# Optimization experiments

Measured on AMD Instinct MI355X. Metric: run time of the kernel, lower is better.

The kernel has to match this reference:

```python
import jax, jax.numpy as jnp
import numpy as np

N = 40000; E = 500000; IN = 128; ED = 16; HID = 64; HEADS = 4; OUT = 256; B = 128
NEG = 0.2  # GATv2 leaky_relu negative slope


def _add_self_loops(edge_index, edge_attr, n):
    # PyG add_self_loops with fill_value='mean': loop attr = mean of incoming edge attrs per node
    dst = edge_index[1]
    s = jax.ops.segment_sum(edge_attr, dst, num_segments=n)
    c = jax.ops.segment_sum(jnp.ones((edge_attr.shape[0],), edge_attr.dtype), dst, num_segments=n)
    loop_attr = s / jnp.maximum(c, 1.0)[:, None]
    loops = jnp.arange(n, dtype=edge_index.dtype)
    ei = jnp.concatenate([edge_index, jnp.stack([loops, loops])], axis=1)
    ea = jnp.concatenate([edge_attr, loop_attr], axis=0)
    return ei, ea


def _seg_softmax(logits, seg, n):
    m = jax.ops.segment_max(logits, seg, num_segments=n)
    m = jnp.where(jnp.isfinite(m), m, 0.0)  # guard empty segments
    e = jnp.exp(logits - m[seg])
    z = jax.ops.segment_sum(e, seg, num_segments=n)
    return e / (z[seg] + 1e-16)


def _gatv2(x, src, dst, ea, Wl, bl, Wr, br, We, att, bias, heads, oc, concat):
    n = x.shape[0]
    xl = (x @ Wl + bl).reshape(n, heads, oc)  # lin_l (source/message transform)
    xr = (x @ Wr + br).reshape(n, heads, oc)  # lin_r (target transform)
    ef = (ea @ We).reshape(-1, heads, oc)     # lin_edge (no bias)
    s = jax.nn.leaky_relu(xl[src] + xr[dst] + ef, NEG)  # [Etot,H,C]
    alpha = _seg_softmax(jnp.einsum('ehc,hc->eh', s, att), dst, n)  # scatter-softmax over dst
    out = jax.ops.segment_sum(xl[src] * alpha[..., None], dst, num_segments=n)  # [N,H,C]
    out = out.reshape(n, heads * oc) if concat else out.mean(axis=1)
    return out + bias


def setup_inputs():
    ks = jax.random.split(jax.random.key(0), 32)
    W = lambda i, shp: jax.random.normal(ks[i], shp, jnp.float32) * 0.05
    z = lambda d: jnp.zeros((d,), jnp.float32)
    H = HEADS * HID
    return dict(
        x=jax.random.normal(ks[0], (N, IN), jnp.float32),
        edge_index=jax.random.randint(ks[1], (2, E), 0, N),
        edge_attr=jax.random.normal(ks[2], (E, ED), jnp.float32),
        batch=jnp.sort(jax.random.randint(ks[3], (N,), 0, B)),
        batch_size=B,
        c1_Wl=W(4, (IN, H)), c1_bl=z(H), c1_Wr=W(5, (IN, H)), c1_br=z(H), c1_We=W(6, (ED, H)), c1_att=W(7, (HEADS, HID)), c1_bias=z(H),
        c2_Wl=W(8, (H, H)), c2_bl=z(H), c2_Wr=W(9, (H, H)), c2_br=z(H), c2_We=W(10, (ED, H)), c2_att=W(11, (HEADS, HID)), c2_bias=z(H),
        c3_Wl=W(12, (H, OUT)), c3_bl=z(OUT), c3_Wr=W(13, (H, OUT)), c3_br=z(OUT), c3_We=W(14, (ED, OUT)), c3_att=W(15, (1, OUT)), c3_bias=z(OUT),
        gate_W1=W(16, (OUT, 128)), gate_b1=z(128), gate_W2=W(17, (128, 1)), gate_b2=z(1),
        reg_W1=W(18, (OUT, 128)), reg_b1=z(128), reg_W2=W(19, (128, 2)), reg_b2=z(2),
    )


def reference(x, edge_index, edge_attr, batch, batch_size,
              c1_Wl, c1_bl, c1_Wr, c1_br, c1_We, c1_att, c1_bias,
              c2_Wl, c2_bl, c2_Wr, c2_br, c2_We, c2_att, c2_bias,
              c3_Wl, c3_bl, c3_Wr, c3_br, c3_We, c3_att, c3_bias,
              gate_W1, gate_b1, gate_W2, gate_b2,
              reg_W1, reg_b1, reg_W2, reg_b2):
    # task_type='homo_lumo' path; dropout disabled (inference)
    ei, ea = _add_self_loops(edge_index, edge_attr, N)
    src, dst = ei[0], ei[1]
    h = jax.nn.relu(_gatv2(x, src, dst, ea, c1_Wl, c1_bl, c1_Wr, c1_br, c1_We, c1_att, c1_bias, HEADS, HID, True))
    h = jax.nn.relu(_gatv2(h, src, dst, ea, c2_Wl, c2_bl, c2_Wr, c2_br, c2_We, c2_att, c2_bias, HEADS, HID, True))
    h = _gatv2(h, src, dst, ea, c3_Wl, c3_bl, c3_Wr, c3_br, c3_We, c3_att, c3_bias, 1, OUT, True)
    # AttentionalAggregation pooling
    gate = jax.nn.relu(h @ gate_W1 + gate_b1) @ gate_W2 + gate_b2  # [N,1]
    a = _seg_softmax(gate[:, 0], batch, batch_size)
    g = jax.ops.segment_sum(h * a[:, None], batch, num_segments=batch_size)  # [B,OUT]
    return jax.nn.relu(g @ reg_W1 + reg_b1) @ reg_W2 + reg_b2  # [B,2]
```

## Files before the change

kernel.cpp:

```cpp
#include <hip/hip_runtime.h>
#include <math.h>

constexpr int N_NODES = 40000;
constexpr int N_EDGES = 500000;
constexpr int ETOT    = N_EDGES + N_NODES;
constexpr int IN_DIM  = 128;
constexpr int ED_DIM  = 16;
constexpr int FEAT    = 256;
constexpr int BATCH   = 128;
constexpr float NEG   = 0.2f;
constexpr int NCHUNK  = (N_NODES + 255) / 256;

typedef __bf16 bf16x8 __attribute__((ext_vector_type(8)));
typedef float  f32x4  __attribute__((ext_vector_type(4)));

__global__ __launch_bounds__(256) void k_deg(const int* __restrict__ dst, int* __restrict__ deg)
{
    int e = blockIdx.x * 256 + threadIdx.x;
    if (e >= ETOT) return;
    int v = e < N_EDGES ? dst[e] : e - N_EDGES;
    atomicAdd(&deg[v], 1);
}

__global__ __launch_bounds__(256) void k_scan1(const int* __restrict__ deg, int* __restrict__ bsum)
{
    __shared__ int s[256];
    int t = threadIdx.x;
    int idx = blockIdx.x * 256 + t;
    s[t] = idx < N_NODES ? deg[idx] : 0;
    __syncthreads();
    for (int st = 128; st; st >>= 1) { if (t < st) s[t] += s[t + st]; __syncthreads(); }
    if (t == 0) bsum[blockIdx.x] = s[0];
}

__global__ __launch_bounds__(256) void k_scan2(const int* __restrict__ bsum,
    int* __restrict__ boff, int* __restrict__ rowptr)
{
    __shared__ int s[256];
    int t = threadIdx.x;
    int v = t < NCHUNK ? bsum[t] : 0;
    s[t] = v;
    __syncthreads();
    for (int off = 1; off < 256; off <<= 1) {
        int x = (t >= off) ? s[t - off] : 0;
        __syncthreads();
        s[t] += x;
        __syncthreads();
    }
    if (t < NCHUNK) boff[t] = s[t] - v;
    if (t == 0) rowptr[N_NODES] = ETOT;
}

__global__ __launch_bounds__(256) void k_scan3(const int* __restrict__ deg,
    const int* __restrict__ boff, int* __restrict__ rowptr)
{
    __shared__ int s[256];
    int t = threadIdx.x;
    int idx = blockIdx.x * 256 + t;
    int v = idx < N_NODES ? deg[idx] : 0;
    s[t] = v;
    __syncthreads();
    for (int off = 1; off < 256; off <<= 1) {
        int x = (t >= off) ? s[t - off] : 0;
        __syncthreads();
        s[t] += x;
        __syncthreads();
    }
    if (idx < N_NODES) rowptr[idx] = boff[blockIdx.x] + s[t] - v;
}

__global__ __launch_bounds__(256) void k_fill(const int* __restrict__ srcA, const int* __restrict__ dst,
    const int* __restrict__ rowptr, int* __restrict__ fill, int2* __restrict__ elist2)
{
    int e = blockIdx.x * 256 + threadIdx.x;
    if (e >= ETOT) return;
    int v = e < N_EDGES ? dst[e]  : e - N_EDGES;
    int s = e < N_EDGES ? srcA[e] : e - N_EDGES;
    int pos = rowptr[v] + atomicAdd(&fill[v], 1);
    elist2[pos] = make_int2(s, e);
}

__global__ __launch_bounds__(256) void k_loop_csr(const int2* __restrict__ elist2,
    const int* __restrict__ rowptr, const float* __restrict__ ea, float* __restrict__ loop_attr)
{
    int t = blockIdx.x * 256 + threadIdx.x;
    if (t >= N_NODES * ED_DIM) return;
    int n = t >> 4, d = t & 15;
    int p0 = rowptr[n], p1 = rowptr[n + 1];
    float s = 0.f; int c = 0;
    for (int p = p0; p < p1; ++p) {
        int e = elist2[p].y;
        if (e < N_EDGES) { s += ea[(size_t)e * ED_DIM + d]; ++c; }
    }
    loop_attr[t] = s / (float)(c > 0 ? c : 1);
}

__device__ __forceinline__ void bsplit(float x, unsigned short& h, unsigned short& l)
{
    unsigned u = __float_as_uint(x);
    unsigned r = (u + 0x7FFFu + ((u >> 16) & 1u)) >> 16;
    h = (unsigned short)r;
    float rem = x - __uint_as_float(r << 16);
    unsigned u2 = __float_as_uint(rem);
    l = (unsigned short)((u2 + 0x7FFFu + ((u2 >> 16) & 1u)) >> 16);
}

__global__ __launch_bounds__(256) void k_cvt(const float* __restrict__ X,
    unsigned short* __restrict__ Xh, unsigned short* __restrict__ Xl, int n4)
{
    int i = blockIdx.x * 256 + threadIdx.x;
    if (i >= n4) return;
    float4 v = ((const float4*)X)[i];
    ushort4 h, l;
    bsplit(v.x, h.x, l.x);
    bsplit(v.y, h.y, l.y);
    bsplit(v.z, h.z, l.z);
    bsplit(v.w, h.w, l.w);
    ((ushort4*)Xh)[i] = h;
    ((ushort4*)Xl)[i] = l;
}

__global__ __launch_bounds__(256) void k_cvtT(const float* __restrict__ W,
    unsigned short* __restrict__ WhT, unsigned short* __restrict__ WlT, int K, int N)
{
    int i = blockIdx.x * 256 + threadIdx.x;
    if (i >= K * N) return;
    int k = i / N, n = i - k * N;
    unsigned short h, l;
    bsplit(W[i], h, l);
    WhT[(size_t)n * K + k] = h;
    WlT[(size_t)n * K + k] = l;
}


__device__ __forceinline__ void stage16(const unsigned short* g, void* lds)
{
#if __has_builtin(__builtin_amdgcn_global_load_lds)
    __builtin_amdgcn_global_load_lds(
        (const __attribute__((address_space(1))) void*)g,
        (__attribute__((address_space(3))) void*)lds, 16, 0, 0);
#else
    ((uint4*)lds)[threadIdx.x & 63] = *(const uint4*)g;
#endif
}

__global__ __launch_bounds__(256) void k_mgemm(
    const unsigned short* __restrict__ Ah, const unsigned short* __restrict__ Al,
    const unsigned short* __restrict__ BhT, const unsigned short* __restrict__ BlT,
    const float* __restrict__ bias, float* __restrict__ C,
    int M, int N, int K, int act)
{
    __shared__ uint4 sAh[512], sAl[512], sBh[512], sBl[512];

    int t = threadIdx.x;
    int lane = t & 63;
    int w = t >> 6;
    int mh = w >> 1, nh = w & 1;
    int bm = blockIdx.x * 128, bn = blockIdx.y * 128;
    int q = lane >> 4, lm = lane & 15;

    int ar0 = bm + w * 16 + lm;        ar0 = ar0 < M ? ar0 : M - 1;
    int ar1 = bm + (w + 4) * 16 + lm;  ar1 = ar1 < M ? ar1 : M - 1;
    int bc0 = bn + w * 16 + lm;
    int bc1 = bn + (w + 4) * 16 + lm;
    size_t aoff0 = (size_t)ar0 * K + q * 8;
    size_t aoff1 = (size_t)ar1 * K + q * 8;
    size_t boff0 = (size_t)bc0 * K + q * 8;
    size_t boff1 = (size_t)bc1 * K + q * 8;

    f32x4 acc[4][4] = {};

    int nk = K >> 5;
    for (int ks = 0; ks < nk; ++ks) {
        int k0 = ks << 5;
        if (ks) __syncthreads();
        stage16(Ah  + aoff0 + k0, &sAh[w * 64]);
        stage16(Ah  + aoff1 + k0, &sAh[(w + 4) * 64]);
        stage16(Al  + aoff0 + k0, &sAl[w * 64]);
        stage16(Al  + aoff1 + k0, &sAl[(w + 4) * 64]);
        stage16(BhT + boff0 + k0, &sBh[w * 64]);
        stage16(BhT + boff1 + k0, &sBh[(w + 4) * 64]);
        stage16(BlT + boff0 + k0, &sBl[w * 64]);
        stage16(BlT + boff1 + k0, &sBl[(w + 4) * 64]);
        __syncthreads();

        bf16x8 fah[4], fal[4], fbh[4], fbl[4];
        #pragma unroll
        for (int mt = 0; mt < 4; ++mt) {
            fah[mt] = __builtin_bit_cast(bf16x8, sAh[(mh * 4 + mt) * 64 + lane]);
            fal[mt] = __builtin_bit_cast(bf16x8, sAl[(mh * 4 + mt) * 64 + lane]);
        }
        #pragma unroll
        for (int nt = 0; nt < 4; ++nt) {
            fbh[nt] = __builtin_bit_cast(bf16x8, sBh[(nh * 4 + nt) * 64 + lane]);
            fbl[nt] = __builtin_bit_cast(bf16x8, sBl[(nh * 4 + nt) * 64 + lane]);
        }
        #pragma unroll
        for (int mt = 0; mt < 4; ++mt)
            #pragma unroll
            for (int nt = 0; nt < 4; ++nt) {
                acc[mt][nt] = __builtin_amdgcn_mfma_f32_16x16x32_bf16(fah[mt], fbh[nt], acc[mt][nt], 0, 0, 0);
                acc[mt][nt] = __builtin_amdgcn_mfma_f32_16x16x32_bf16(fah[mt], fbl[nt], acc[mt][nt], 0, 0, 0);
                acc[mt][nt] = __builtin_amdgcn_mfma_f32_16x16x32_bf16(fal[mt], fbh[nt], acc[mt][nt], 0, 0, 0);
            }
    }

    #pragma unroll
    for (int nt = 0; nt < 4; ++nt) {
        int col = bn + nh * 64 + nt * 16 + lm;
        float bb = bias[col];
        #pragma unroll
        for (int mt = 0; mt < 4; ++mt) {
            #pragma unroll
            for (int i = 0; i < 4; ++i) {
                int row = bm + mh * 64 + mt * 16 + q * 4 + i;
                if (row < M) {
                    float o = acc[mt][nt][i] + bb;
                    if (act) o = fmaxf(o, 0.f);
                    C[(size_t)row * N + col] = o;
                }
            }
        }
    }
}

static void launch_mgemm(const unsigned short* Ah, const unsigned short* Al,
                         const unsigned short* BhT, const unsigned short* BlT,
                         const float* bias, float* C, int M, int N, int K, int act,
                         hipStream_t stream)
{
    dim3 grid((M + 127) / 128, N / 128);
    k_mgemm<<<grid, 256, 0, stream>>>(Ah, Al, BhT, BlT, bias, C, M, N, K, act);
}

#define XELOAD(s) do {                                                                \
    int src_ = __builtin_amdgcn_readfirstlane(eS[s].x);                               \
    int e_   = __builtin_amdgcn_readfirstlane(eS[s].y);                               \
    const float4* eb4_ = reinterpret_cast<const float4*>(                             \
        (e_ < N_EDGES) ? ea + (size_t)e_ * ED_DIM                                     \
                       : loop_attr + (size_t)src_ * ED_DIM);                          \
    evS[s][0] = eb4_[0]; evS[s][1] = eb4_[1];                                         \
    evS[s][2] = eb4_[2]; evS[s][3] = eb4_[3];                                         \
    xlvS[s] = *(const float4*)(xl + (size_t)src_ * FEAT + base);                      \
} while (0)

#define COMPUTE(s) do {                                                               \
    float ef0_ = 0.f, ef1_ = 0.f, ef2_ = 0.f, ef3_ = 0.f;                             \
    const float* ed_ = (const float*)evS[s];                                          \
    _Pragma("unroll")                                                                 \
    for (int d_ = 0; d_ < ED_DIM; ++d_) {                                             \
        float a_ = ed_[d_];                                                           \
        ef0_ = fmaf(a_, weR[d_].x, ef0_); ef1_ = fmaf(a_, weR[d_].y, ef1_);           \
        ef2_ = fmaf(a_, weR[d_].z, ef2_); ef3_ = fmaf(a_, weR[d_].w, ef3_);           \
    }                                                                                 \
    float s0_ = xlvS[s].x + xrv.x + ef0_;                                             \
    float s1_ = xlvS[s].y + xrv.y + ef1_;                                             \
    float s2_ = xlvS[s].z + xrv.z + ef2_;                                             \
    float s3_ = xlvS[s].w + xrv.w + ef3_;                                             \
    s0_ = fmaxf(s0_, 0.f) + NEG * fminf(s0_, 0.f);                                    \
    s1_ = fmaxf(s1_, 0.f) + NEG * fminf(s1_, 0.f);                                    \
    s2_ = fmaxf(s2_, 0.f) + NEG * fminf(s2_, 0.f);                                    \
    s3_ = fmaxf(s3_, 0.f) + NEG * fminf(s3_, 0.f);                                    \
    float l_ = fmaf(s0_, attR.x, fmaf(s1_, attR.y, fmaf(s2_, attR.z, s3_ * attR.w))); \
    l_ += __shfl_xor(l_, 1, 64);                                                      \
    l_ += __shfl_xor(l_, 2, 64);                                                      \
    l_ += __shfl_xor(l_, 4, 64);                                                      \
    l_ += __shfl_xor(l_, 8, 64);                                                      \
    if (H == 1) { l_ += __shfl_xor(l_, 16, 64); l_ += __shfl_xor(l_, 32, 64); }       \
    float nm_ = fmaxf(m, l_);                                                         \
    float sc_ = __expf(m - nm_);                                                      \
    float w_  = __expf(l_ - nm_);                                                     \
    z = fmaf(z, sc_, w_);                                                             \
    m = nm_;                                                                          \
    acc.x = fmaf(acc.x, sc_, w_ * xlvS[s].x);                                         \
    acc.y = fmaf(acc.y, sc_, w_ * xlvS[s].y);                                         \
    acc.z = fmaf(acc.z, sc_, w_ * xlvS[s].z);                                         \
    acc.w = fmaf(acc.w, sc_, w_ * xlvS[s].w);                                         \
} while (0)

template <int H, int RELU, int OUTMODE>
__global__ __launch_bounds__(256, 4) void k_gat(
    const float* __restrict__ xl, const float* __restrict__ xr,
    const float* __restrict__ ea, const float* __restrict__ loop_attr,
    const int2* __restrict__ elist2, const int* __restrict__ rowptr,
    const float* __restrict__ We, const float* __restrict__ att,
    const float* __restrict__ bias, float* __restrict__ out,
    unsigned short* __restrict__ outH, unsigned short* __restrict__ outL)
{
    int t = threadIdx.x;
    int lane = t & 63;
    int n = __builtin_amdgcn_readfirstlane(blockIdx.x * 4 + (t >> 6));
    int base = lane * 4;

    float4 weR[ED_DIM];
    #pragma unroll
    for (int d = 0; d < ED_DIM; ++d)
        weR[d] = *(const float4*)(We + d * FEAT + base);

    float4 attR = *(const float4*)(att + base);
    float4 xrv  = *(const float4*)(xr + (size_t)n * FEAT + base);

    float m = -INFINITY, z = 0.f;
    float4 acc = {0.f, 0.f, 0.f, 0.f};

    int p0 = rowptr[n], p1 = rowptr[n + 1];
    int pe = p1 - 1;

    int2   eS[2];
    float4 evS[2][4];
    float4 xlvS[2];

    eS[0] = elist2[p0];
    { int pc = p0 + 1 > pe ? pe : p0 + 1; eS[1] = elist2[pc]; }
    XELOAD(0);

    int p = p0;
    while (true) {
        XELOAD(1);
        { int pn = p + 2 > pe ? pe : p + 2; eS[0] = elist2[pn]; }
        COMPUTE(0);
        if (++p >= p1) break;
        XELOAD(0);
        { int pn = p + 2 > pe ? pe : p + 2; eS[1] = elist2[pn]; }
        COMPUTE(1);
        if (++p >= p1) break;
    }

    float inv = 1.0f / (z + 1e-16f);
    float4 bs = *(const float4*)(bias + base);
    float4 o;
    o.x = fmaf(acc.x, inv, bs.x);
    o.y = fmaf(acc.y, inv, bs.y);
    o.z = fmaf(acc.z, inv, bs.z);
    o.w = fmaf(acc.w, inv, bs.w);
    if (RELU) {
        o.x = fmaxf(o.x, 0.f); o.y = fmaxf(o.y, 0.f);
        o.z = fmaxf(o.z, 0.f); o.w = fmaxf(o.w, 0.f);
    }
    if (OUTMODE == 2)
        *(float4*)(out + (size_t)n * FEAT + base) = o;
    ushort4 oh, ol;
    bsplit(o.x, oh.x, ol.x);
    bsplit(o.y, oh.y, ol.y);
    bsplit(o.z, oh.z, ol.z);
    bsplit(o.w, oh.w, ol.w);
    *(ushort4*)(outH + (size_t)n * FEAT + base) = oh;
    *(ushort4*)(outL + (size_t)n * FEAT + base) = ol;
}

__global__ __launch_bounds__(256) void k_gate_score(const float* __restrict__ ghid,
    const float* __restrict__ W2, const float* __restrict__ b2, float* __restrict__ gate)
{
    int lane = threadIdx.x & 63;
    int n = blockIdx.x * 4 + (threadIdx.x >> 6);
    float v = ghid[(size_t)n * 128 + lane] * W2[lane] + ghid[(size_t)n * 128 + lane + 64] * W2[lane + 64];
    #pragma unroll
    for (int off = 32; off > 0; off >>= 1) v += __shfl_xor(v, off, 64);
    if (lane == 0) gate[n] = v + b2[0];
}

__device__ __forceinline__ int lbound(const int* a, int n, int v)
{
    int lo = 0, hi = n;
    while (lo < hi) { int mid = (lo + hi) >> 1; if (a[mid] < v) lo = mid + 1; else hi = mid; }
    return lo;
}

__global__ __launch_bounds__(256) void k_pool(const float* __restrict__ gate,
    const float* __restrict__ h, const int* __restrict__ batch, float* __restrict__ g)
{
    int b = blockIdx.x;
    int t = threadIdx.x;
    __shared__ float red[256];
    int start = lbound(batch, N_NODES, b);
    int end   = lbound(batch, N_NODES, b + 1);

    float mx = -INFINITY;
    for (int n = start + t; n < end; n += 256) mx = fmaxf(mx, gate[n]);
    red[t] = mx; __syncthreads();
    for (int s = 128; s; s >>= 1) { if (t < s) red[t] = fmaxf(red[t], red[t + s]); __syncthreads(); }
    float m = red[0];
    __syncthreads();

    float zs = 0.f;
    for (int n = start + t; n < end; n += 256) zs += __expf(gate[n] - m);
    red[t] = zs; __syncthreads();
    for (int s = 128; s; s >>= 1) { if (t < s) red[t] += red[t + s]; __syncthreads(); }
    float z = red[0];

    float gs = 0.f;
    for (int n = start; n < end; ++n) gs += __expf(gate[n] - m) * h[(size_t)n * FEAT + t];
    g[b * FEAT + t] = gs / (z + 1e-16f);
}

__global__ __launch_bounds__(128) void k_reg(const float* __restrict__ g,
    const float* __restrict__ W1, const float* __restrict__ b1,
    const float* __restrict__ W2, const float* __restrict__ b2, float* __restrict__ out)
{
    int b = blockIdx.x, t = threadIdx.x;
    __shared__ float sg[FEAT];
    sg[t] = g[b * FEAT + t];
    sg[t + 128] = g[b * FEAT + t + 128];
    __syncthreads();
    float hv = b1[t];
    for (int k = 0; k < FEAT; ++k) hv += sg[k] * W1[k * 128 + t];
    hv = fmaxf(hv, 0.f);
    __shared__ float p0s[128], p1s[128];
    p0s[t] = hv * W2[t * 2 + 0];
    p1s[t] = hv * W2[t * 2 + 1];
    __syncthreads();
    for (int s = 64; s; s >>= 1) {
        if (t < s) { p0s[t] += p0s[t + s]; p1s[t] += p1s[t + s]; }
        __syncthreads();
    }
    if (t == 0) { out[b * 2 + 0] = p0s[0] + b2[0]; out[b * 2 + 1] = p1s[0] + b2[1]; }
}

extern "C" void kernel_launch(void* const* d_in, const int* in_sizes, int n_in,
                              void* d_out, int out_size, void* d_ws, size_t ws_size,
                              hipStream_t stream)
{
    const float* x       = (const float*)d_in[0];
    const int*   ei      = (const int*)d_in[1];
    const float* ea      = (const float*)d_in[2];
    const int*   batch   = (const int*)d_in[3];
    const float* c1_Wl   = (const float*)d_in[5];
    const float* c1_bl   = (const float*)d_in[6];
    const float* c1_Wr   = (const float*)d_in[7];
    const float* c1_br   = (const float*)d_in[8];
    const float* c1_We   = (const float*)d_in[9];
    const float* c1_att  = (const float*)d_in[10];
    const float* c1_bias = (const float*)d_in[11];
    const float* c2_Wl   = (const float*)d_in[12];
    const float* c2_bl   = (const float*)d_in[13];
    const float* c2_Wr   = (const float*)d_in[14];
    const float* c2_br   = (const float*)d_in[15];
    const float* c2_We   = (const float*)d_in[16];
    const float* c2_att  = (const float*)d_in[17];
    const float* c2_bias = (const float*)d_in[18];
    const float* c3_Wl   = (const float*)d_in[19];
    const float* c3_bl   = (const float*)d_in[20];
    const float* c3_Wr   = (const float*)d_in[21];
    const float* c3_br   = (const float*)d_in[22];
    const float* c3_We   = (const float*)d_in[23];
    const float* c3_att  = (const float*)d_in[24];
    const float* c3_bias = (const float*)d_in[25];
    const float* gate_W1 = (const float*)d_in[26];
    const float* gate_b1 = (const float*)d_in[27];
    const float* gate_W2 = (const float*)d_in[28];
    const float* gate_b2 = (const float*)d_in[29];
    const float* reg_W1  = (const float*)d_in[30];
    const float* reg_b1  = (const float*)d_in[31];
    const float* reg_W2  = (const float*)d_in[32];
    const float* reg_b2  = (const float*)d_in[33];

    const int* srcArr = ei;
    const int* dstArr = ei + N_EDGES;

    float* ws = (float*)d_ws;
    size_t off = 0;
    auto alloc = [&](size_t nf) { float* p = ws + off; off += (nf + 63) & ~(size_t)63; return p; };
    float* xl        = alloc((size_t)N_NODES * FEAT);
    float* xr        = alloc((size_t)N_NODES * FEAT);
    float* h         = alloc((size_t)N_NODES * FEAT);
    float* loop_attr = alloc((size_t)N_NODES * ED_DIM);
    float* gpool     = alloc((size_t)BATCH * FEAT);
    unsigned short* Ah = (unsigned short*)alloc((size_t)N_NODES * FEAT / 2);
    unsigned short* Al = (unsigned short*)alloc((size_t)N_NODES * FEAT / 2);
    unsigned short* wlT_h = (unsigned short*)alloc(FEAT * FEAT / 2);
    unsigned short* wlT_l = (unsigned short*)alloc(FEAT * FEAT / 2);
    unsigned short* wrT_h = (unsigned short*)alloc(FEAT * FEAT / 2);
    unsigned short* wrT_l = (unsigned short*)alloc(FEAT * FEAT / 2);
    int* ibase  = (int*)(ws + off);
    int* deg    = ibase;
    int* fill   = ibase + N_NODES;
    int* rowptr = ibase + 2 * N_NODES;
    int* bsum   = ibase + 3 * N_NODES + 64;
    int* boff   = bsum + 256;
    int2* elist2 = (int2*)(boff + 256);

    float* ghid = xl;
    float* gate = xr;

    hipMemsetAsync(deg, 0, (size_t)2 * N_NODES * sizeof(int), stream);

    k_deg<<<(ETOT + 255) / 256, 256, 0, stream>>>(dstArr, deg);
    k_scan1<<<NCHUNK, 256, 0, stream>>>(deg, bsum);
    k_scan2<<<1, 256, 0, stream>>>(bsum, boff, rowptr);
    k_scan3<<<NCHUNK, 256, 0, stream>>>(deg, boff, rowptr);
    k_fill<<<(ETOT + 255) / 256, 256, 0, stream>>>(srcArr, dstArr, rowptr, fill, elist2);
    k_loop_csr<<<(N_NODES * ED_DIM + 255) / 256, 256, 0, stream>>>(elist2, rowptr, ea, loop_attr);

    {
        int n4 = N_NODES * IN_DIM / 4;
        k_cvt<<<(n4 + 255) / 256, 256, 0, stream>>>(x, Ah, Al, n4);
        k_cvtT<<<(IN_DIM * FEAT + 255) / 256, 256, 0, stream>>>(c1_Wl, wlT_h, wlT_l, IN_DIM, FEAT);
        k_cvtT<<<(IN_DIM * FEAT + 255) / 256, 256, 0, stream>>>(c1_Wr, wrT_h, wrT_l, IN_DIM, FEAT);
        launch_mgemm(Ah, Al, wlT_h, wlT_l, c1_bl, xl, N_NODES, FEAT, IN_DIM, 0, stream);
        launch_mgemm(Ah, Al, wrT_h, wrT_l, c1_br, xr, N_NODES, FEAT, IN_DIM, 0, stream);
    }
    k_gat<4, 1, 1><<<N_NODES / 4, 256, 0, stream>>>(xl, xr, ea, loop_attr, elist2, rowptr,
                                                    c1_We, c1_att, c1_bias, h, Ah, Al);
    {
        k_cvtT<<<(FEAT * FEAT + 255) / 256, 256, 0, stream>>>(c2_Wl, wlT_h, wlT_l, FEAT, FEAT);
        k_cvtT<<<(FEAT * FEAT + 255) / 256, 256, 0, stream>>>(c2_Wr, wrT_h, wrT_l, FEAT, FEAT);
        launch_mgemm(Ah, Al, wlT_h, wlT_l, c2_bl, xl, N_NODES, FEAT, FEAT, 0, stream);
        launch_mgemm(Ah, Al, wrT_h, wrT_l, c2_br, xr, N_NODES, FEAT, FEAT, 0, stream);
    }
    k_gat<4, 1, 1><<<N_NODES / 4, 256, 0, stream>>>(xl, xr, ea, loop_attr, elist2, rowptr,
                                                    c2_We, c2_att, c2_bias, h, Ah, Al);
    {
        k_cvtT<<<(FEAT * FEAT + 255) / 256, 256, 0, stream>>>(c3_Wl, wlT_h, wlT_l, FEAT, FEAT);
        k_cvtT<<<(FEAT * FEAT + 255) / 256, 256, 0, stream>>>(c3_Wr, wrT_h, wrT_l, FEAT, FEAT);
        launch_mgemm(Ah, Al, wlT_h, wlT_l, c3_bl, xl, N_NODES, FEAT, FEAT, 0, stream);
        launch_mgemm(Ah, Al, wrT_h, wrT_l, c3_br, xr, N_NODES, FEAT, FEAT, 0, stream);
    }
    k_gat<1, 0, 2><<<N_NODES / 4, 256, 0, stream>>>(xl, xr, ea, loop_attr, elist2, rowptr,
                                                    c3_We, c3_att, c3_bias, h, Ah, Al);

    {
        k_cvtT<<<(FEAT * 128 + 255) / 256, 256, 0, stream>>>(gate_W1, wlT_h, wlT_l, FEAT, 128);
        launch_mgemm(Ah, Al, wlT_h, wlT_l, gate_b1, ghid, N_NODES, 128, FEAT, 1, stream);
    }
    k_gate_score<<<N_NODES / 4, 256, 0, stream>>>(ghid, gate_W2, gate_b2, gate);
    k_pool<<<BATCH, 256, 0, stream>>>(gate, h, batch, gpool);
    k_reg<<<BATCH, 128, 0, stream>>>(gpool, reg_W1, reg_b1, reg_W2, reg_b2, (float*)d_out);
}
```

Baseline: 1.037 ms.

## Split GAT heads across two waves per node and shrink GEMM M-tile to 64

Adds a k_gat2 kernel for the 4-head layers in which each node's 256 features are split across two waves, each lane handling 2 features. This doubles the number of waves walking each edge list so more gather loads are in flight, and it drops the unused fp32 h write. The GEMM tile is halved in M (64x128) to launch more blocks and improve CU occupancy, at the cost of more B-tile reloads. The single-head layer 3 keeps the old kernel, now specialized without template parameters.

```diff
diff --git a/kernel.cpp b/kernel.cpp
--- a/kernel.cpp
+++ b/kernel.cpp
@@ -132,7 +132,6 @@
     WlT[(size_t)n * K + k] = l;
 }
 
-
 __device__ __forceinline__ void stage16(const unsigned short* g, void* lds)
 {
 #if __has_builtin(__builtin_amdgcn_global_load_lds)
@@ -150,45 +149,41 @@
     const float* __restrict__ bias, float* __restrict__ C,
     int M, int N, int K, int act)
 {
-    __shared__ uint4 sAh[512], sAl[512], sBh[512], sBl[512];
+    __shared__ uint4 sAh[256], sAl[256], sBh[512], sBl[512];
 
     int t = threadIdx.x;
     int lane = t & 63;
     int w = t >> 6;
     int mh = w >> 1, nh = w & 1;
-    int bm = blockIdx.x * 128, bn = blockIdx.y * 128;
+    int bm = blockIdx.x * 64, bn = blockIdx.y * 128;
     int q = lane >> 4, lm = lane & 15;
 
-    int ar0 = bm + w * 16 + lm;        ar0 = ar0 < M ? ar0 : M - 1;
-    int ar1 = bm + (w + 4) * 16 + lm;  ar1 = ar1 < M ? ar1 : M - 1;
-    int bc0 = bn + w * 16 + lm;
-    int bc1 = bn + (w + 4) * 16 + lm;
-    size_t aoff0 = (size_t)ar0 * K + q * 8;
-    size_t aoff1 = (size_t)ar1 * K + q * 8;
+    int ar = bm + w * 16 + lm;  ar = ar < M ? ar : M - 1;
+    int bc0 = bn + (2 * w) * 16 + lm;
+    int bc1 = bn + (2 * w + 1) * 16 + lm;
+    size_t aoff  = (size_t)ar * K + q * 8;
     size_t boff0 = (size_t)bc0 * K + q * 8;
     size_t boff1 = (size_t)bc1 * K + q * 8;
 
-    f32x4 acc[4][4] = {};
+    f32x4 acc[2][4] = {};
 
     int nk = K >> 5;
     for (int ks = 0; ks < nk; ++ks) {
         int k0 = ks << 5;
         if (ks) __syncthreads();
-        stage16(Ah  + aoff0 + k0, &sAh[w * 64]);
-        stage16(Ah  + aoff1 + k0, &sAh[(w + 4) * 64]);
-        stage16(Al  + aoff0 + k0, &sAl[w * 64]);
-        stage16(Al  + aoff1 + k0, &sAl[(w + 4) * 64]);
-        stage16(BhT + boff0 + k0, &sBh[w * 64]);
-        stage16(BhT + boff1 + k0, &sBh[(w + 4) * 64]);
-        stage16(BlT + boff0 + k0, &sBl[w * 64]);
-        stage16(BlT + boff1 + k0, &sBl[(w + 4) * 64]);
+        stage16(Ah  + aoff  + k0, &sAh[w * 64]);
+        stage16(Al  + aoff  + k0, &sAl[w * 64]);
+        stage16(BhT + boff0 + k0, &sBh[(2 * w) * 64]);
+        stage16(BhT + boff1 + k0, &sBh[(2 * w + 1) * 64]);
+        stage16(BlT + boff0 + k0, &sBl[(2 * w) * 64]);
+        stage16(BlT + boff1 + k0, &sBl[(2 * w + 1) * 64]);
         __syncthreads();
 
-        bf16x8 fah[4], fal[4], fbh[4], fbl[4];
+        bf16x8 fah[2], fal[2], fbh[4], fbl[4];
         #pragma unroll
-        for (int mt = 0; mt < 4; ++mt) {
-            fah[mt] = __builtin_bit_cast(bf16x8, sAh[(mh * 4 + mt) * 64 + lane]);
-            fal[mt] = __builtin_bit_cast(bf16x8, sAl[(mh * 4 + mt) * 64 + lane]);
+        for (int mt = 0; mt < 2; ++mt) {
+            fah[mt] = __builtin_bit_cast(bf16x8, sAh[(mh * 2 + mt) * 64 + lane]);
+            fal[mt] = __builtin_bit_cast(bf16x8, sAl[(mh * 2 + mt) * 64 + lane]);
         }
         #pragma unroll
         for (int nt = 0; nt < 4; ++nt) {
@@ -196,7 +191,7 @@
             fbl[nt] = __builtin_bit_cast(bf16x8, sBl[(nh * 4 + nt) * 64 + lane]);
         }
         #pragma unroll
-        for (int mt = 0; mt < 4; ++mt)
+        for (int mt = 0; mt < 2; ++mt)
             #pragma unroll
             for (int nt = 0; nt < 4; ++nt) {
                 acc[mt][nt] = __builtin_amdgcn_mfma_f32_16x16x32_bf16(fah[mt], fbh[nt], acc[mt][nt], 0, 0, 0);
@@ -210,10 +205,10 @@
         int col = bn + nh * 64 + nt * 16 + lm;
         float bb = bias[col];
         #pragma unroll
-        for (int mt = 0; mt < 4; ++mt) {
+        for (int mt = 0; mt < 2; ++mt) {
             #pragma unroll
             for (int i = 0; i < 4; ++i) {
-                int row = bm + mh * 64 + mt * 16 + q * 4 + i;
+                int row = bm + mh * 32 + mt * 16 + q * 4 + i;
                 if (row < M) {
                     float o = acc[mt][nt][i] + bb;
                     if (act) o = fmaxf(o, 0.f);
@@ -229,8 +224,106 @@
                          const float* bias, float* C, int M, int N, int K, int act,
                          hipStream_t stream)
 {
-    dim3 grid((M + 127) / 128, N / 128);
+    dim3 grid((M + 63) / 64, N / 128);
     k_mgemm<<<grid, 256, 0, stream>>>(Ah, Al, BhT, BlT, bias, C, M, N, K, act);
+}
+
+#define G2_XELOAD(s) do {                                                             \
+    int src_ = __builtin_amdgcn_readfirstlane(eS[s].x);                               \
+    int e_   = __builtin_amdgcn_readfirstlane(eS[s].y);                               \
+    const float4* eb4_ = reinterpret_cast<const float4*>(                             \
+        (e_ < N_EDGES) ? ea + (size_t)e_ * ED_DIM                                     \
+                       : loop_attr + (size_t)src_ * ED_DIM);                          \
+    evS[s][0] = eb4_[0]; evS[s][1] = eb4_[1];                                         \
+    evS[s][2] = eb4_[2]; evS[s][3] = eb4_[3];                                         \
+    xlvS[s] = *(const float2*)(xl + (size_t)src_ * FEAT + base);                      \
+} while (0)
+
+#define G2_COMPUTE(s) do {                                                            \
+    float ef0_ = 0.f, ef1_ = 0.f;                                                     \
+    const float* ed_ = (const float*)evS[s];                                          \
+    _Pragma("unroll")                                                                 \
+    for (int d_ = 0; d_ < ED_DIM; ++d_) {                                             \
+        float a_ = ed_[d_];                                                           \
+        ef0_ = fmaf(a_, weR[d_].x, ef0_); ef1_ = fmaf(a_, weR[d_].y, ef1_);           \
+    }                                                                                 \
+    float s0_ = xlvS[s].x + xrv.x + ef0_;                                             \
+    float s1_ = xlvS[s].y + xrv.y + ef1_;                                             \
+    s0_ = fmaxf(s0_, 0.f) + NEG * fminf(s0_, 0.f);                                    \
+    s1_ = fmaxf(s1_, 0.f) + NEG * fminf(s1_, 0.f);                                    \
+    float l_ = fmaf(s0_, attR.x, s1_ * attR.y);                                       \
+    l_ += __shfl_xor(l_, 1, 64);                                                      \
+    l_ += __shfl_xor(l_, 2, 64);                                                      \
+    l_ += __shfl_xor(l_, 4, 64);                                                      \
+    l_ += __shfl_xor(l_, 8, 64);                                                      \
+    l_ += __shfl_xor(l_, 16, 64);                                                     \
+    float nm_ = fmaxf(m, l_);                                                         \
+    float sc_ = __expf(m - nm_);                                                      \
+    float w_  = __expf(l_ - nm_);                                                     \
+    z = fmaf(z, sc_, w_);                                                             \
+    m = nm_;                                                                          \
+    acc.x = fmaf(acc.x, sc_, w_ * xlvS[s].x);                                         \
+    acc.y = fmaf(acc.y, sc_, w_ * xlvS[s].y);                                         \
+} while (0)
+
+__global__ __launch_bounds__(256, 4) void k_gat2(
+    const float* __restrict__ xl, const float* __restrict__ xr,
+    const float* __restrict__ ea, const float* __restrict__ loop_attr,
+    const int2* __restrict__ elist2, const int* __restrict__ rowptr,
+    const float* __restrict__ We, const float* __restrict__ att,
+    const float* __restrict__ bias,
+    unsigned short* __restrict__ outH, unsigned short* __restrict__ outL)
+{
+    int t = threadIdx.x;
+    int lane = t & 63;
+    int w = t >> 6;
+    int half = w & 1;
+    int n = __builtin_amdgcn_readfirstlane(blockIdx.x * 2 + (w >> 1));
+    int base = half * 128 + lane * 2;
+
+    float2 weR[ED_DIM];
+    #pragma unroll
+    for (int d = 0; d < ED_DIM; ++d)
+        weR[d] = *(const float2*)(We + d * FEAT + base);
+
+    float2 attR = *(const float2*)(att + base);
+    float2 xrv  = *(const float2*)(xr + (size_t)n * FEAT + base);
+
+    float m = -INFINITY, z = 0.f;
+    float2 acc = {0.f, 0.f};
+
+    int p0 = rowptr[n], p1 = rowptr[n + 1];
+    int pe = p1 - 1;
+
+    int2   eS[2];
+    float4 evS[2][4];
+    float2 xlvS[2];
+
+    eS[0] = elist2[p0];
+    { int pc = p0 + 1 > pe ? pe : p0 + 1; eS[1] = elist2[pc]; }
+    G2_XELOAD(0);
+
+    int p = p0;
+    while (true) {
+        G2_XELOAD(1);
+        { int pn = p + 2 > pe ? pe : p + 2; eS[0] = elist2[pn]; }
+        G2_COMPUTE(0);
+        if (++p >= p1) break;
+        G2_XELOAD(0);
+        { int pn = p + 2 > pe ? pe : p + 2; eS[1] = elist2[pn]; }
+        G2_COMPUTE(1);
+        if (++p >= p1) break;
+    }
+
+    float inv = 1.0f / (z + 1e-16f);
+    float2 bs = *(const float2*)(bias + base);
+    float ox = fmaxf(fmaf(acc.x, inv, bs.x), 0.f);
+    float oy = fmaxf(fmaf(acc.y, inv, bs.y), 0.f);
+    ushort2 oh, ol;
+    bsplit(ox, oh.x, ol.x);
+    bsplit(oy, oh.y, ol.y);
+    *(ushort2*)(outH + (size_t)n * FEAT + base) = oh;
+    *(ushort2*)(outL + (size_t)n * FEAT + base) = ol;
 }
 
 #define XELOAD(s) do {                                                                \
@@ -266,7 +359,8 @@
     l_ += __shfl_xor(l_, 2, 64);                                                      \
     l_ += __shfl_xor(l_, 4, 64);                                                      \
     l_ += __shfl_xor(l_, 8, 64);                                                      \
-    if (H == 1) { l_ += __shfl_xor(l_, 16, 64); l_ += __shfl_xor(l_, 32, 64); }       \
+    l_ += __shfl_xor(l_, 16, 64);                                                     \
+    l_ += __shfl_xor(l_, 32, 64);                                                     \
     float nm_ = fmaxf(m, l_);                                                         \
     float sc_ = __expf(m - nm_);                                                      \
     float w_  = __expf(l_ - nm_);                                                     \
@@ -278,8 +372,7 @@
     acc.w = fmaf(acc.w, sc_, w_ * xlvS[s].w);                                         \
 } while (0)
 
-template <int H, int RELU, int OUTMODE>
-__global__ __launch_bounds__(256, 4) void k_gat(
+__global__ __launch_bounds__(256, 4) void k_gat1(
     const float* __restrict__ xl, const float* __restrict__ xr,
     const float* __restrict__ ea, const float* __restrict__ loop_attr,
     const int2* __restrict__ elist2, const int* __restrict__ rowptr,
@@ -333,12 +426,7 @@
     o.y = fmaf(acc.y, inv, bs.y);
     o.z = fmaf(acc.z, inv, bs.z);
     o.w = fmaf(acc.w, inv, bs.w);
-    if (RELU) {
-        o.x = fmaxf(o.x, 0.f); o.y = fmaxf(o.y, 0.f);
-        o.z = fmaxf(o.z, 0.f); o.w = fmaxf(o.w, 0.f);
-    }
-    if (OUTMODE == 2)
-        *(float4*)(out + (size_t)n * FEAT + base) = o;
+    *(float4*)(out + (size_t)n * FEAT + base) = o;
     ushort4 oh, ol;
     bsplit(o.x, oh.x, ol.x);
     bsplit(o.y, oh.y, ol.y);
@@ -499,24 +587,24 @@
         launch_mgemm(Ah, Al, wlT_h, wlT_l, c1_bl, xl, N_NODES, FEAT, IN_DIM, 0, stream);
         launch_mgemm(Ah, Al, wrT_h, wrT_l, c1_br, xr, N_NODES, FEAT, IN_DIM, 0, stream);
     }
-    k_gat<4, 1, 1><<<N_NODES / 4, 256, 0, stream>>>(xl, xr, ea, loop_attr, elist2, rowptr,
-                                                    c1_We, c1_att, c1_bias, h, Ah, Al);
+    k_gat2<<<N_NODES / 2, 256, 0, stream>>>(xl, xr, ea, loop_attr, elist2, rowptr,
+                                            c1_We, c1_att, c1_bias, Ah, Al);
     {
         k_cvtT<<<(FEAT * FEAT + 255) / 256, 256, 0, stream>>>(c2_Wl, wlT_h, wlT_l, FEAT, FEAT);
         k_cvtT<<<(FEAT * FEAT + 255) / 256, 256, 0, stream>>>(c2_Wr, wrT_h, wrT_l, FEAT, FEAT);
         launch_mgemm(Ah, Al, wlT_h, wlT_l, c2_bl, xl, N_NODES, FEAT, FEAT, 0, stream);
         launch_mgemm(Ah, Al, wrT_h, wrT_l, c2_br, xr, N_NODES, FEAT, FEAT, 0, stream);
     }
-    k_gat<4, 1, 1><<<N_NODES / 4, 256, 0, stream>>>(xl, xr, ea, loop_attr, elist2, rowptr,
-                                                    c2_We, c2_att, c2_bias, h, Ah, Al);
+    k_gat2<<<N_NODES / 2, 256, 0, stream>>>(xl, xr, ea, loop_attr, elist2, rowptr,
+                                            c2_We, c2_att, c2_bias, Ah, Al);
     {
         k_cvtT<<<(FEAT * FEAT + 255) / 256, 256, 0, stream>>>(c3_Wl, wlT_h, wlT_l, FEAT, FEAT);
         k_cvtT<<<(FEAT * FEAT + 255) / 256, 256, 0, stream>>>(c3_Wr, wrT_h, wrT_l, FEAT, FEAT);
         launch_mgemm(Ah, Al, wlT_h, wlT_l, c3_bl, xl, N_NODES, FEAT, FEAT, 0, stream);
         launch_mgemm(Ah, Al, wrT_h, wrT_l, c3_br, xr, N_NODES, FEAT, FEAT, 0, stream);
     }
-    k_gat<1, 0, 2><<<N_NODES / 4, 256, 0, stream>>>(xl, xr, ea, loop_attr, elist2, rowptr,
-                                                    c3_We, c3_att, c3_bias, h, Ah, Al);
+    k_gat1<<<N_NODES / 4, 256, 0, stream>>>(xl, xr, ea, loop_attr, elist2, rowptr,
+                                            c3_We, c3_att, c3_bias, h, Ah, Al);
 
     {
         k_cvtT<<<(FEAT * 128 + 255) / 256, 256, 0, stream>>>(gate_W1, wlT_h, wlT_l, FEAT, 128);
```

Result: no change. 1.055 ms (+1.7%).
